# Kernel tuning notes

Hardware: AMD Instinct MI355X
Metric: run time of the kernel (lower is better)

The kernel has to match this reference:

```python
import jax, jax.numpy as jnp
import numpy as np

EPS = 1e-5

def _gn(x, w, b):
    # GroupNorm with 1 group on [N, C]: normalize each row over C, then affine.
    mu = jnp.mean(x, axis=-1, keepdims=True)
    var = jnp.mean((x - mu) ** 2, axis=-1, keepdims=True)
    return (x - mu) * jax.lax.rsqrt(var + EPS) * w + b

def setup_inputs() -> dict:
    key = jax.random.key(0)
    ks = jax.random.split(key, 24)
    N_AGT, N_CTX, E, D, NC = 50000, 100000, 500000, 128, 2
    s = 0.05  # weight init scale
    inp = {
        "agts": jax.random.normal(ks[0], (N_AGT, D), jnp.float32),
        "ctx": jax.random.normal(ks[1], (N_CTX, D), jnp.float32),
        "agt_ctrs": jax.random.normal(ks[2], (N_AGT, NC), jnp.float32),
        "ctx_ctrs": jax.random.normal(ks[3], (N_CTX, NC), jnp.float32),
        "hi": jax.random.randint(ks[4], (E,), 0, N_AGT, jnp.int32),
        "wi": jax.random.randint(ks[5], (E,), 0, N_CTX, jnp.int32),
        # dist MLP: Linear(2->128, bias) + ReLU, then Linear(128->128 no bias)+GN+ReLU
        "Wd1": jax.random.normal(ks[6], (D, NC), jnp.float32) * s,
        "bd1": jnp.zeros((D,), jnp.float32),
        "Wd2": jax.random.normal(ks[7], (D, D), jnp.float32) * s,
        "gd2w": jnp.ones((D,), jnp.float32), "gd2b": jnp.zeros((D,), jnp.float32),
        # query: Linear(128->128 no bias)+GN+ReLU
        "Wq": jax.random.normal(ks[8], (D, D), jnp.float32) * s,
        "gqw": jnp.ones((D,), jnp.float32), "gqb": jnp.zeros((D,), jnp.float32),
        # ctx MLP: Linear(384->128 no bias)+GN+ReLU, then Linear(128->128 no bias)
        "Wc1": jax.random.normal(ks[9], (D, 3 * D), jnp.float32) * s,
        "gc1w": jnp.ones((D,), jnp.float32), "gc1b": jnp.zeros((D,), jnp.float32),
        "Wc2": jax.random.normal(ks[10], (D, D), jnp.float32) * s,
        # agt linear (no bias), post-scatter GN, final Linear(no bias)+GN
        "Wa": jax.random.normal(ks[11], (D, D), jnp.float32) * s,
        "gnw": jnp.ones((D,), jnp.float32), "gnb": jnp.zeros((D,), jnp.float32),
        "Wl": jax.random.normal(ks[12], (D, D), jnp.float32) * s,
        "glw": jnp.ones((D,), jnp.float32), "glb": jnp.zeros((D,), jnp.float32),
    }
    return inp

def reference(agts, ctx, agt_ctrs, ctx_ctrs, hi, wi,
              Wd1, bd1, Wd2, gd2w, gd2b, Wq, gqw, gqb,
              Wc1, gc1w, gc1b, Wc2, Wa, gnw, gnb, Wl, glw, glb):
    res = agts
    # dist branch: relative center offsets of edges -> MLP
    d = agt_ctrs[hi] - ctx_ctrs[wi]                    # [E, 2]
    d = jax.nn.relu(d @ Wd1.T + bd1)                   # [E, 128]
    d = jax.nn.relu(_gn(d @ Wd2.T, gd2w, gd2b))        # [E, 128]
    # query branch: gathered agent features
    q = jax.nn.relu(_gn(agts[hi] @ Wq.T, gqw, gqb))    # [E, 128]
    # ctx branch: concat(dist, query, gathered ctx) -> MLP
    c = jnp.concatenate([d, q, ctx[wi]], axis=1)       # [E, 384]
    c = jax.nn.relu(_gn(c @ Wc1.T, gc1w, gc1b))        # [E, 128]
    c = c @ Wc2.T                                      # [E, 128]
    # scatter-add messages back to agents
    a = agts @ Wa.T
    a = a.at[hi].add(c)
    a = jax.nn.relu(_gn(a, gnw, gnb))
    a = _gn(a @ Wl.T, glw, glb)
    return jax.nn.relu(a + res)
```

## Files before the change

### kernel.cpp

```cpp
#include <hip/hip_runtime.h>
#include <hip/hip_bf16.h>

#define D 128
#define TM 64
#define APITCH 136

typedef __attribute__((ext_vector_type(8))) short short8;
typedef __attribute__((ext_vector_type(4))) float f32x4;
typedef __attribute__((ext_vector_type(2))) float f32x2;

__device__ __forceinline__ short f2bf(float f) {
    union { float f; unsigned u; } v; v.f = f;
    unsigned r = v.u + 0x7fffu + ((v.u >> 16) & 1u);
    return (short)(r >> 16);
}

struct TileLDS {
    short A[TM * APITCH];
    f32x2 red[TM][4][4];
    f32x2 mr[TM];
    int hi_s[TM];
    int wi_s[TM];
};

__device__ __forceinline__ short8 load_bfrag(const float* p) {
    short8 r;
#pragma unroll
    for (int j = 0; j < 8; ++j) r[j] = f2bf(p[j]);
    return r;
}

__device__ __forceinline__ void load_wset(const float* W, int pitch, int n0, int lr, int kh,
                                          short8 frag[2][4]) {
#pragma unroll
    for (int t = 0; t < 2; ++t)
#pragma unroll
        for (int ks = 0; ks < 4; ++ks)
            frag[t][ks] = load_bfrag(W + (size_t)(n0 + t * 16 + lr) * pitch + ks * 32 + kh * 8);
}

__device__ __forceinline__ void wave_gemm(const short* A, const short8 frag[2][4],
                                          int lr, int kh, f32x4 acc[4][2]) {
#pragma unroll
    for (int mt = 0; mt < 4; ++mt)
#pragma unroll
        for (int t = 0; t < 2; ++t)
            acc[mt][t] = (f32x4){0.f, 0.f, 0.f, 0.f};
#pragma unroll
    for (int ks = 0; ks < 4; ++ks) {
        short8 a[4];
#pragma unroll
        for (int mt = 0; mt < 4; ++mt)
            a[mt] = *(const short8*)&A[(mt * 16 + lr) * APITCH + ks * 32 + kh * 8];
#pragma unroll
        for (int mt = 0; mt < 4; ++mt)
#pragma unroll
            for (int t = 0; t < 2; ++t)
                acc[mt][t] = __builtin_amdgcn_mfma_f32_16x16x32_bf16(a[mt], frag[t][ks], acc[mt][t], 0, 0, 0);
    }
}

__device__ __forceinline__ void store_acc_global(float* Y, long rbase, int M,
                                                 const f32x4 acc[4][2], int lane, int w) {
    int lr = lane & 15, hh = lane >> 4;
#pragma unroll
    for (int mt = 0; mt < 4; ++mt)
#pragma unroll
        for (int t = 0; t < 2; ++t)
#pragma unroll
            for (int r = 0; r < 4; ++r) {
                int row = mt * 16 + hh * 4 + r;
                if (rbase + row < M)
                    Y[(size_t)(rbase + row) * D + w * 32 + t * 16 + lr] = acc[mt][t][r];
            }
}

__device__ __forceinline__ void gn_stats(TileLDS& L, const f32x4 acc[4][2],
                                         int tid, int lane, int w) {
    int lr = lane & 15, hh = lane >> 4;
#pragma unroll
    for (int mt = 0; mt < 4; ++mt)
#pragma unroll
        for (int r = 0; r < 4; ++r) {
            float s = acc[mt][0][r] + acc[mt][1][r];
            float q = acc[mt][0][r] * acc[mt][0][r] + acc[mt][1][r] * acc[mt][1][r];
            s += __shfl_xor(s, 1); q += __shfl_xor(q, 1);
            s += __shfl_xor(s, 2); q += __shfl_xor(q, 2);
            if ((lr & 3) == mt) {
                int row = mt * 16 + hh * 4 + r;
                L.red[row][w][lr >> 2] = (f32x2){s, q};
            }
        }
    __syncthreads();
    if (tid < TM) {
        float s = 0.f, q = 0.f;
        const f32x2* p = (const f32x2*)L.red[tid];
#pragma unroll
        for (int i = 0; i < 16; ++i) { f32x2 v = p[i]; s += v[0]; q += v[1]; }
        float mu = s * (1.f / 128.f);
        float var = q * (1.f / 128.f) - mu * mu;
        L.mr[tid] = (f32x2){mu, rsqrtf(var + 1e-5f)};
    }
    __syncthreads();
}

__device__ __forceinline__ void gn_reg(TileLDS& L, const f32x4 acc[4][2],
                                       float gw0, float gb0, float gw1, float gb1,
                                       int tid, int lane, int w) {
    gn_stats(L, acc, tid, lane, w);
    int lr = lane & 15, hh = lane >> 4, n0 = w * 32;
#pragma unroll
    for (int mt = 0; mt < 4; ++mt)
#pragma unroll
        for (int r = 0; r < 4; ++r) {
            int row = mt * 16 + hh * 4 + r;
            f32x2 m = L.mr[row];
            float v0 = (acc[mt][0][r] - m[0]) * m[1] * gw0 + gb0;
            float v1 = (acc[mt][1][r] - m[0]) * m[1] * gw1 + gb1;
            L.A[row * APITCH + n0 + lr]      = f2bf(fmaxf(v0, 0.f));
            L.A[row * APITCH + n0 + 16 + lr] = f2bf(fmaxf(v1, 0.f));
        }
    __syncthreads();
}

__device__ __forceinline__ void stage_rows_to_A(TileLDS& L, const float* X, long rbase, int M, int tid) {
#pragma unroll
    for (int it = 0; it < 8; ++it) {
        int chunk = tid + it * 256;
        int row = chunk >> 5, c4 = chunk & 31;
        long r = rbase + row;
        float4 v = (r < M) ? *(const float4*)&X[(size_t)r * D + c4 * 4] : make_float4(0.f, 0.f, 0.f, 0.f);
        short* a = &L.A[row * APITCH + c4 * 4];
        a[0] = f2bf(v.x); a[1] = f2bf(v.y); a[2] = f2bf(v.z); a[3] = f2bf(v.w);
    }
}

__global__ __launch_bounds__(256, 3)
void k_qpath(const float* __restrict__ agts,
             const float* __restrict__ Wq, const float* __restrict__ gqw, const float* __restrict__ gqb,
             const float* __restrict__ Wc1, const float* __restrict__ Wa,
             float* __restrict__ qpart, float* __restrict__ abuf, int M, int ntiles) {
    __shared__ TileLDS L;
    int tid = threadIdx.x;
    int lane = tid & 63, w = tid >> 6;
    int lr = lane & 15, kh = lane >> 4;
    int n0 = w * 32;
    short8 fa[2][4], fq[2][4], fcq[2][4];
    load_wset(Wa, 128, n0, lr, kh, fa);
    load_wset(Wq, 128, n0, lr, kh, fq);
    load_wset(Wc1 + 128, 384, n0, lr, kh, fcq);
    float gw0 = gqw[n0 + lr], gw1 = gqw[n0 + 16 + lr];
    float gb0 = gqb[n0 + lr], gb1 = gqb[n0 + 16 + lr];

    for (int tile = blockIdx.x; tile < ntiles; tile += gridDim.x) {
        long rbase = (long)tile * TM;
        stage_rows_to_A(L, agts, rbase, M, tid);
        __syncthreads();
        f32x4 acc[4][2];
        wave_gemm(L.A, fa, lr, kh, acc);
        store_acc_global(abuf, rbase, M, acc, lane, w);
        wave_gemm(L.A, fq, lr, kh, acc);
        gn_reg(L, acc, gw0, gb0, gw1, gb1, tid, lane, w);
        wave_gemm(L.A, fcq, lr, kh, acc);
        store_acc_global(qpart, rbase, M, acc, lane, w);
        __syncthreads();
    }
}

__global__ __launch_bounds__(256, 4)
void k_ctx(const float* __restrict__ ctx, const float* __restrict__ Wc1,
           float* __restrict__ cpart, int M, int ntiles) {
    __shared__ TileLDS L;
    int tid = threadIdx.x;
    int lane = tid & 63, w = tid >> 6;
    int lr = lane & 15, kh = lane >> 4;
    short8 fc[2][4];
    load_wset(Wc1 + 256, 384, w * 32, lr, kh, fc);
    for (int tile = blockIdx.x; tile < ntiles; tile += gridDim.x) {
        long rbase = (long)tile * TM;
        stage_rows_to_A(L, ctx, rbase, M, tid);
        __syncthreads();
        f32x4 acc[4][2];
        wave_gemm(L.A, fc, lr, kh, acc);
        store_acc_global(cpart, rbase, M, acc, lane, w);
        __syncthreads();
    }
}

__global__ __launch_bounds__(256, 3)
void k_edge(const float* __restrict__ agt_ctrs, const float* __restrict__ ctx_ctrs,
            const int* __restrict__ hi, const int* __restrict__ wi,
            const float* __restrict__ Wd1, const float* __restrict__ bd1,
            const float* __restrict__ Wd2, const float* __restrict__ gd2w, const float* __restrict__ gd2b,
            const float* __restrict__ Wc1, const float* __restrict__ gc1w, const float* __restrict__ gc1b,
            const float* __restrict__ Wc2,
            const float* __restrict__ qpart, const float* __restrict__ cpart,
            float* __restrict__ abuf, int E, int ntiles) {
    __shared__ TileLDS L;
    int tid = threadIdx.x;
    int lane = tid & 63, w = tid >> 6;
    int lr = lane & 15, kh = lane >> 4;
    int n0 = w * 32;
    short8 fd2[2][4], fc1[2][4], fc2[2][4];
    load_wset(Wd2, 128, n0, lr, kh, fd2);
    load_wset(Wc1, 384, n0, lr, kh, fc1);
    load_wset(Wc2, 128, n0, lr, kh, fc2);
    float g2w0 = gd2w[n0 + lr], g2w1 = gd2w[n0 + 16 + lr];
    float g2b0 = gd2b[n0 + lr], g2b1 = gd2b[n0 + 16 + lr];
    float g1w0 = gc1w[n0 + lr], g1w1 = gc1w[n0 + 16 + lr];
    float g1b0 = gc1b[n0 + lr], g1b1 = gc1b[n0 + 16 + lr];

    for (int tile = blockIdx.x; tile < ntiles; tile += gridDim.x) {
        long ebase = (long)tile * TM;
        if (tid < TM) {
            long e = ebase + tid;
            L.hi_s[tid] = (e < E) ? hi[e] : 0;
            L.wi_s[tid] = (e < E) ? wi[e] : 0;
        }
        {
            int row = tid >> 2, q4 = tid & 3;
            long e = ebase + row;
            bool valid = e < E;
            float dd0 = 0.f, dd1 = 0.f;
            if (valid) {
                int h = hi[e], c = wi[e];
                dd0 = agt_ctrs[h * 2 + 0] - ctx_ctrs[c * 2 + 0];
                dd1 = agt_ctrs[h * 2 + 1] - ctx_ctrs[c * 2 + 1];
            }
#pragma unroll
            for (int cb = 0; cb < 4; ++cb) {
                short8 ov;
#pragma unroll
                for (int j = 0; j < 8; ++j) {
                    int c = q4 * 32 + cb * 8 + j;
                    float v = valid ? fmaxf(Wd1[c * 2 + 0] * dd0 + Wd1[c * 2 + 1] * dd1 + bd1[c], 0.f) : 0.f;
                    ov[j] = f2bf(v);
                }
                *(short8*)&L.A[row * APITCH + q4 * 32 + cb * 8] = ov;
            }
        }
        __syncthreads();
        f32x4 acc[4][2];
        wave_gemm(L.A, fd2, lr, kh, acc);
        gn_reg(L, acc, g2w0, g2b0, g2w1, g2b1, tid, lane, w);
        wave_gemm(L.A, fc1, lr, kh, acc);
#pragma unroll
        for (int mt = 0; mt < 4; ++mt)
#pragma unroll
            for (int r = 0; r < 4; ++r) {
                int row = mt * 16 + kh * 4 + r;
                const float* qp = qpart + (size_t)L.hi_s[row] * D;
                const float* cp = cpart + (size_t)L.wi_s[row] * D;
                acc[mt][0][r] += qp[n0 + lr]      + cp[n0 + lr];
                acc[mt][1][r] += qp[n0 + 16 + lr] + cp[n0 + 16 + lr];
            }
        gn_reg(L, acc, g1w0, g1b0, g1w1, g1b1, tid, lane, w);
        wave_gemm(L.A, fc2, lr, kh, acc);
#pragma unroll
        for (int mt = 0; mt < 4; ++mt)
#pragma unroll
            for (int r = 0; r < 4; ++r) {
                int erow = mt * 16 + kh * 4 + r;
                long e = ebase + erow;
                if (e < E) {
                    size_t base = (size_t)L.hi_s[erow] * D;
                    atomicAdd(&abuf[base + n0 + lr],      acc[mt][0][r]);
                    atomicAdd(&abuf[base + n0 + 16 + lr], acc[mt][1][r]);
                }
            }
        __syncthreads();
    }
}

__global__ __launch_bounds__(256, 4)
void k_final(const float* __restrict__ abuf, const float* __restrict__ agts,
             const float* __restrict__ Wl,
             const float* __restrict__ gnw, const float* __restrict__ gnb,
             const float* __restrict__ glw, const float* __restrict__ glb,
             float* __restrict__ out, int M, int ntiles) {
    __shared__ TileLDS L;
    int tid = threadIdx.x;
    int lane = tid & 63, w = tid >> 6;
    int lr = lane & 15, kh = lane >> 4;
    int n0 = w * 32;
    short8 fl[2][4];
    load_wset(Wl, 128, n0, lr, kh, fl);
    float gw0 = glw[n0 + lr], gw1 = glw[n0 + 16 + lr];
    float gb0 = glb[n0 + lr], gb1 = glb[n0 + 16 + lr];

    for (int tile = blockIdx.x; tile < ntiles; tile += gridDim.x) {
        long rbase = (long)tile * TM;
        int row = tid >> 2, q4 = tid & 3;
        long r = rbase + row;
        float x[32];
        {
            float s = 0.f, q = 0.f;
            const float4* src = (const float4*)(abuf + (size_t)r * D + q4 * 32);
#pragma unroll
            for (int i = 0; i < 8; ++i) {
                float4 v = (r < M) ? src[i] : make_float4(0.f, 0.f, 0.f, 0.f);
                x[i * 4 + 0] = v.x; x[i * 4 + 1] = v.y; x[i * 4 + 2] = v.z; x[i * 4 + 3] = v.w;
                s += v.x + v.y + v.z + v.w;
                q += v.x * v.x + v.y * v.y + v.z * v.z + v.w * v.w;
            }
            L.red[row][q4][0] = (f32x2){s, q};
        }
        __syncthreads();
        if (tid < TM) {
            float s = 0.f, q = 0.f;
#pragma unroll
            for (int i = 0; i < 4; ++i) { f32x2 v = L.red[tid][i][0]; s += v[0]; q += v[1]; }
            float mu = s * (1.f / 128.f);
            float var = q * (1.f / 128.f) - mu * mu;
            L.mr[tid] = (f32x2){mu, rsqrtf(var + 1e-5f)};
        }
        __syncthreads();
        {
            f32x2 m = L.mr[row];
#pragma unroll
            for (int cb = 0; cb < 4; ++cb) {
                short8 ov;
#pragma unroll
                for (int j = 0; j < 8; ++j) {
                    int c = q4 * 32 + cb * 8 + j;
                    float v = (x[cb * 8 + j] - m[0]) * m[1] * gnw[c] + gnb[c];
                    ov[j] = f2bf(fmaxf(v, 0.f));
                }
                *(short8*)&L.A[row * APITCH + q4 * 32 + cb * 8] = ov;
            }
        }
        __syncthreads();
        f32x4 acc[4][2];
        wave_gemm(L.A, fl, lr, kh, acc);
        gn_stats(L, acc, tid, lane, w);
#pragma unroll
        for (int mt = 0; mt < 4; ++mt)
#pragma unroll
            for (int rr = 0; rr < 4; ++rr) {
                int orow = mt * 16 + kh * 4 + rr;
                long gr = rbase + orow;
                if (gr < M) {
                    f32x2 m = L.mr[orow];
                    float v0 = (acc[mt][0][rr] - m[0]) * m[1] * gw0 + gb0;
                    float v1 = (acc[mt][1][rr] - m[0]) * m[1] * gw1 + gb1;
                    v0 += agts[(size_t)gr * D + n0 + lr];
                    v1 += agts[(size_t)gr * D + n0 + 16 + lr];
                    out[(size_t)gr * D + n0 + lr]      = fmaxf(v0, 0.f);
                    out[(size_t)gr * D + n0 + 16 + lr] = fmaxf(v1, 0.f);
                }
            }
        __syncthreads();
    }
}

extern "C" void kernel_launch(void* const* d_in, const int* in_sizes, int n_in,
                              void* d_out, int out_size, void* d_ws, size_t ws_size,
                              hipStream_t stream) {
    const float* agts     = (const float*)d_in[0];
    const float* ctx      = (const float*)d_in[1];
    const float* agt_ctrs = (const float*)d_in[2];
    const float* ctx_ctrs = (const float*)d_in[3];
    const int*   hi       = (const int*)d_in[4];
    const int*   wi       = (const int*)d_in[5];
    const float* Wd1 = (const float*)d_in[6];
    const float* bd1 = (const float*)d_in[7];
    const float* Wd2 = (const float*)d_in[8];
    const float* gd2w = (const float*)d_in[9];
    const float* gd2b = (const float*)d_in[10];
    const float* Wq  = (const float*)d_in[11];
    const float* gqw = (const float*)d_in[12];
    const float* gqb = (const float*)d_in[13];
    const float* Wc1 = (const float*)d_in[14];
    const float* gc1w = (const float*)d_in[15];
    const float* gc1b = (const float*)d_in[16];
    const float* Wc2 = (const float*)d_in[17];
    const float* Wa  = (const float*)d_in[18];
    const float* gnw = (const float*)d_in[19];
    const float* gnb = (const float*)d_in[20];
    const float* Wl  = (const float*)d_in[21];
    const float* glw = (const float*)d_in[22];
    const float* glb = (const float*)d_in[23];

    int N_AGT = in_sizes[0] / D;
    int N_CTX = in_sizes[1] / D;
    int E     = in_sizes[4];
    float* out = (float*)d_out;

    float* qpart = (float*)d_ws;
    float* cpart = qpart + (size_t)N_AGT * D;
    float* abuf  = cpart + (size_t)N_CTX * D;

    int tq = (N_AGT + TM - 1) / TM;
    int tc = (N_CTX + TM - 1) / TM;
    int te = (E + TM - 1) / TM;

    k_qpath<<<tq, 256, 0, stream>>>(agts, Wq, gqw, gqb, Wc1, Wa, qpart, abuf, N_AGT, tq);
    k_ctx<<<tc, 256, 0, stream>>>(ctx, Wc1, cpart, N_CTX, tc);
    k_edge<<<te, 256, 0, stream>>>(agt_ctrs, ctx_ctrs, hi, wi, Wd1, bd1,
                                   Wd2, gd2w, gd2b, Wc1, gc1w, gc1b, Wc2,
                                   qpart, cpart, abuf, E, te);
    k_final<<<tq, 256, 0, stream>>>(abuf, agts, Wl, gnw, gnb, glw, glb, out, N_AGT, tq);
}
```

Measured before the change: 1.023 ms.

## Replace per-edge atomic scatter with CSR-sorted gather of bf16 edge messages

Builds a CSR index of edges grouped by destination agent (histogram, single-block scan, fill), has the edge kernel write its per-edge messages to a bf16 buffer, and adds a gather kernel that sums each agent's messages and adds them into abuf. This is meant to remove 64M float atomics on random addresses. In exchange it adds several launches, a serial one-block scan over 50k entries, and a 128 MB bf16 write and re-read. Storing messages in bf16 also loses precision before the sum.

```diff
diff --git a/kernel.cpp b/kernel.cpp
--- a/kernel.cpp
+++ b/kernel.cpp
@@ -13,6 +13,12 @@
     union { float f; unsigned u; } v; v.f = f;
     unsigned r = v.u + 0x7fffu + ((v.u >> 16) & 1u);
     return (short)(r >> 16);
+}
+__device__ __forceinline__ float bflo(unsigned v) {
+    union { unsigned u; float f; } t; t.u = v << 16; return t.f;
+}
+__device__ __forceinline__ float bfhi(unsigned v) {
+    union { unsigned u; float f; } t; t.u = v & 0xffff0000u; return t.f;
 }
 
 struct TileLDS {
@@ -132,6 +138,50 @@
         float4 v = (r < M) ? *(const float4*)&X[(size_t)r * D + c4 * 4] : make_float4(0.f, 0.f, 0.f, 0.f);
         short* a = &L.A[row * APITCH + c4 * 4];
         a[0] = f2bf(v.x); a[1] = f2bf(v.y); a[2] = f2bf(v.z); a[3] = f2bf(v.w);
+    }
+}
+
+__global__ void k_hist(const int* __restrict__ hi, int* __restrict__ cnt, int E) {
+    int i = blockIdx.x * 256 + threadIdx.x;
+    if (i < E) atomicAdd(&cnt[hi[i]], 1);
+}
+
+__global__ void k_scan(const int* __restrict__ cnt, int* __restrict__ offs,
+                       int* __restrict__ cursor, int n) {
+    __shared__ int wsum[4];
+    __shared__ int carry_s;
+    int tid = threadIdx.x, lane = tid & 63, w = tid >> 6;
+    if (tid == 0) carry_s = 0;
+    __syncthreads();
+    for (int base = 0; base < n; base += 256) {
+        int i = base + tid;
+        int v = (i < n) ? cnt[i] : 0;
+        int x = v;
+#pragma unroll
+        for (int d = 1; d < 64; d <<= 1) {
+            int t = __shfl_up(x, d);
+            if (lane >= d) x += t;
+        }
+        if (lane == 63) wsum[w] = x;
+        __syncthreads();
+        int woff = 0;
+        for (int j = 0; j < w; ++j) woff += wsum[j];
+        int carry = carry_s;
+        int excl = carry + woff + x - v;
+        if (i < n) { offs[i] = excl; cursor[i] = excl; }
+        __syncthreads();
+        if (tid == 255) carry_s = carry + woff + x;
+        __syncthreads();
+    }
+    if (tid == 0) offs[n] = carry_s;
+}
+
+__global__ void k_fill(const int* __restrict__ hi, int* __restrict__ cursor,
+                       int* __restrict__ eidx, int E) {
+    int i = blockIdx.x * 256 + threadIdx.x;
+    if (i < E) {
+        int p = atomicAdd(&cursor[hi[i]], 1);
+        eidx[p] = i;
     }
 }
 
@@ -195,7 +245,7 @@
             const float* __restrict__ Wc1, const float* __restrict__ gc1w, const float* __restrict__ gc1b,
             const float* __restrict__ Wc2,
             const float* __restrict__ qpart, const float* __restrict__ cpart,
-            float* __restrict__ abuf, int E, int ntiles) {
+            short* __restrict__ ebuf, int E, int ntiles) {
     __shared__ TileLDS L;
     int tid = threadIdx.x;
     int lane = tid & 63, w = tid >> 6;
@@ -263,13 +313,33 @@
                 int erow = mt * 16 + kh * 4 + r;
                 long e = ebase + erow;
                 if (e < E) {
-                    size_t base = (size_t)L.hi_s[erow] * D;
-                    atomicAdd(&abuf[base + n0 + lr],      acc[mt][0][r]);
-                    atomicAdd(&abuf[base + n0 + 16 + lr], acc[mt][1][r]);
+                    short* dst = ebuf + (size_t)e * D;
+                    dst[n0 + lr]      = f2bf(acc[mt][0][r]);
+                    dst[n0 + 16 + lr] = f2bf(acc[mt][1][r]);
                 }
             }
         __syncthreads();
     }
+}
+
+__global__ __launch_bounds__(256, 8)
+void k_gather(const short* __restrict__ ebuf, const int* __restrict__ offs,
+              const int* __restrict__ eidx, float* __restrict__ abuf, int M) {
+    int w = threadIdx.x >> 6, lane = threadIdx.x & 63;
+    int a = blockIdx.x * 4 + w;
+    if (a >= M) return;
+    int s = offs[a], e1 = offs[a + 1];
+    float s0 = 0.f, s1 = 0.f;
+    for (int p = s; p < e1; ++p) {
+        int e = eidx[p];
+        unsigned v = *(const unsigned*)&ebuf[(size_t)e * D + lane * 2];
+        s0 += bflo(v);
+        s1 += bfhi(v);
+    }
+    float2* dst = (float2*)&abuf[(size_t)a * D + lane * 2];
+    float2 cur = *dst;
+    cur.x += s0; cur.y += s1;
+    *dst = cur;
 }
 
 __global__ __launch_bounds__(256, 4)
@@ -389,15 +459,27 @@
     float* qpart = (float*)d_ws;
     float* cpart = qpart + (size_t)N_AGT * D;
     float* abuf  = cpart + (size_t)N_CTX * D;
+    short* ebuf  = (short*)(abuf + (size_t)N_AGT * D);
+    int*   cnt    = (int*)(ebuf + (size_t)E * D);
+    int*   offs   = cnt + N_AGT;
+    int*   cursor = offs + N_AGT + 1;
+    int*   eidx   = cursor + N_AGT;
 
     int tq = (N_AGT + TM - 1) / TM;
     int tc = (N_CTX + TM - 1) / TM;
     int te = (E + TM - 1) / TM;
+    int ge = (E + 255) / 256;
+
+    hipMemsetAsync(cnt, 0, (size_t)N_AGT * sizeof(int), stream);
+    k_hist<<<ge, 256, 0, stream>>>(hi, cnt, E);
+    k_scan<<<1, 256, 0, stream>>>(cnt, offs, cursor, N_AGT);
+    k_fill<<<ge, 256, 0, stream>>>(hi, cursor, eidx, E);
 
     k_qpath<<<tq, 256, 0, stream>>>(agts, Wq, gqw, gqb, Wc1, Wa, qpart, abuf, N_AGT, tq);
     k_ctx<<<tc, 256, 0, stream>>>(ctx, Wc1, cpart, N_CTX, tc);
     k_edge<<<te, 256, 0, stream>>>(agt_ctrs, ctx_ctrs, hi, wi, Wd1, bd1,
                                    Wd2, gd2w, gd2b, Wc1, gc1w, gc1b, Wc2,
-                                   qpart, cpart, abuf, E, te);
+                                   qpart, cpart, ebuf, E, te);
+    k_gather<<<(N_AGT + 3) / 4, 256, 0, stream>>>(ebuf, offs, eidx, abuf, N_AGT);
     k_final<<<tq, 256, 0, stream>>>(abuf, agts, Wl, gnw, gnb, glw, glb, out, N_AGT, tq);
 }
```

Result: slower. 1.268 ms (+24.0%).
